# Kernel tuning notes

Measured on AMD Instinct MI355X. Metric: run time of the kernel, lower is better.

Reference implementation:

```python
import jax, jax.numpy as jnp
import numpy as np

SLOPE = 0.1  # supar MLP uses LeakyReLU(0.1)

def _mlp(x, W, b):
    return jax.nn.leaky_relu(x @ W + b, negative_slope=SLOPE)

def _triaffine(x, y, z, W):
    # supar Triaffine with n_out=1: s[b,z,x,y] = sum_{i,k,j} x[b,x,i] W[i,k,j] y[b,y,j] z[b,z,k]
    w = jnp.einsum('bzk,ikj->bzij', z, W)          # [b, n, d, d]
    return jnp.einsum('bxi,bzij,byj->bzxy', x, w, y)  # [b, n, n, n]

def _triu_sym(s):
    # s.triu() + s.triu(1).transpose(-1, -2) over last two dims
    return jnp.triu(s) + jnp.swapaxes(jnp.triu(s, 1), -1, -2)

def setup_inputs() -> dict:
    key = jax.random.key(0)
    B, N, D_IN, D = 2, 128, 1024, 150
    ks = jax.random.split(key, 16)
    sc_in = 1.0 / np.sqrt(D_IN)
    sc_tri = float(D) ** -1.5  # keeps triaffine outputs O(1)
    def nrm(k, shape, sc):
        return jax.random.normal(k, shape, jnp.float32) * sc
    return {
        'x':   jax.random.normal(ks[0], (B, N, D_IN), jnp.float32),
        'W_sh': nrm(ks[1], (D_IN, D), sc_in), 'b_sh': jnp.zeros((D,), jnp.float32),
        'W_st': nrm(ks[2], (D_IN, D), sc_in), 'b_st': jnp.zeros((D,), jnp.float32),
        'W_p':  nrm(ks[3], (D_IN, D), sc_in), 'b_p':  jnp.zeros((D,), jnp.float32),
        'T_pt':    nrm(ks[4], (D, D, D), sc_tri),
        'T_ph':    nrm(ks[5], (D, D, D), sc_tri),
        'T_phsib': nrm(ks[6], (D, D, D), sc_tri),
        'T_ptsib': nrm(ks[7], (D, D, D), sc_tri),
        'T_phcop': nrm(ks[8], (D, D, D), sc_tri),
        'T_ptcop': nrm(ks[9], (D, D, D), sc_tri),
    }

def reference(x, W_sh, b_sh, W_st, b_st, W_p, b_p,
              T_pt, T_ph, T_phsib, T_ptsib, T_phcop, T_ptcop):
    # eval mode: dropout is identity; ind_prd=False so p2 == p (shared MLP)
    sh = _mlp(x, W_sh, b_sh)
    st = _mlp(x, W_st, b_st)
    p = _mlp(x, W_p, b_p)
    p2 = p
    # span scores: [b, p, sh_idx, st_idx]
    span_pst = _triu_sym(_triaffine(sh, st, p2, T_pt))
    span_psh = _triaffine(sh, st, p, T_ph)
    # sibling scores: [b, p, h, h'] / [b, p, t, t']
    ph_sib = _triu_sym(_triaffine(sh, sh, p, T_phsib))
    pt_sib = _triu_sym(_triaffine(st, st, p2, T_ptsib))
    # co-parent scores: triaffine gives [b, h, p, p'], permute(0,2,3,1) -> [b, p, p', h]
    ph_cop = jnp.transpose(_triu_sym(_triaffine(p, p, sh, T_phcop)), (0, 2, 3, 1))
    pt_cop = jnp.transpose(_triu_sym(_triaffine(p2, p2, st, T_ptcop)), (0, 2, 3, 1))
    return (span_psh, span_pst, ph_sib, pt_sib, ph_cop, pt_cop)
```

## Files before the change

### kernel.cpp

```cpp
#include <hip/hip_runtime.h>


#define DD    150
#define KP    160
#define OUTBLK 4194304
#define NWZ   24064
#define TTG   3840000
#define WZG   (256*NWZ)
#define HROW  (256*160)

__device__ __forceinline__ unsigned short f2u(float f) {
  unsigned x = __float_as_uint(f);
  x += 0x7FFFu + ((x >> 16) & 1u);
  return (unsigned short)(x >> 16);
}

typedef __attribute__((ext_vector_type(8))) short frag8;
typedef __attribute__((ext_vector_type(4))) float facc4;

__constant__ int c_zsel[6] = {2, 2, 2, 2, 0, 1};
__constant__ int c_xsel[6] = {0, 0, 0, 1, 2, 2};
__constant__ int c_ysel[6] = {1, 1, 0, 1, 2, 2};

__global__ __launch_bounds__(256) void mlp_partial(
    const float* __restrict__ x,
    const float* __restrict__ W0, const float* __restrict__ W1, const float* __restrict__ W2,
    float* __restrict__ P)
{
  int m = blockIdx.x, bt = blockIdx.y, ks = blockIdx.z;
  const float* W = (m == 0) ? W0 : (m == 1) ? W1 : W2;
  int bn0 = bt * 32, k0 = ks * 128;
  __shared__ float xs[32][132];
  int tid = threadIdx.x;
  for (int e = 0; e < 4; ++e) {
    int l = e * 256 + tid;
    int row = l >> 5, c4 = l & 31;
    float4 v = *(const float4*)&x[(bn0 + row) * 1024 + k0 + c4 * 4];
    xs[row][c4 * 4 + 0] = v.x; xs[row][c4 * 4 + 1] = v.y;
    xs[row][c4 * 4 + 2] = v.z; xs[row][c4 * 4 + 3] = v.w;
  }
  __syncthreads();
  int tj = tid & 15, tt = tid >> 4, r = tt * 2;
  int dd[10];
  #pragma unroll
  for (int u = 0; u < 10; ++u) { int d = tj + 16 * u; dd[u] = d < 150 ? d : 149; }
  float a0[10], a1[10];
  #pragma unroll
  for (int u = 0; u < 10; ++u) { a0[u] = 0.f; a1[u] = 0.f; }
  for (int k = 0; k < 128; ++k) {
    float xa = xs[r][k], xb = xs[r + 1][k];
    const float* wr = W + (long long)(k0 + k) * 150;
    #pragma unroll
    for (int u = 0; u < 10; ++u) {
      float w = wr[dd[u]];
      a0[u] += xa * w; a1[u] += xb * w;
    }
  }
  float* Pb = P + (long long)(m * 8 + ks) * 256 * 160;
  #pragma unroll
  for (int u = 0; u < 10; ++u) {
    int d = tj + 16 * u;
    Pb[(bn0 + r) * 160 + d]     = a0[u];
    Pb[(bn0 + r + 1) * 160 + d] = a1[u];
  }
}

__global__ __launch_bounds__(256) void mlp_reduce(
    const float* __restrict__ P,
    const float* __restrict__ B0, const float* __restrict__ B1, const float* __restrict__ B2,
    unsigned short* __restrict__ H)
{
  int o = blockIdx.x * 256 + threadIdx.x;
  int d = o % 160;
  int bn = (o / 160) & 255;
  int m = o / (160 * 256);
  float v = 0.f;
  if (d < 150) {
    const float* Bv = (m == 0) ? B0 : (m == 1) ? B1 : B2;
    v = Bv[d];
    #pragma unroll
    for (int ks = 0; ks < 8; ++ks)
      v += P[((long long)(m * 8 + ks) * 256 + bn) * 160 + d];
    v = v > 0.f ? v : 0.1f * v;
  }
  H[o] = f2u(v);
}

struct TPtrs { const float* t[6]; };
__global__ __launch_bounds__(256) void tt_kernel(TPtrs tp, unsigned short* __restrict__ TT3)
{
  int i = blockIdx.x;
  int ky = blockIdx.y % 5, jy = blockIdx.y / 5;
  int k0 = ky * 32, j0 = jy * 32;
  int g = blockIdx.z;
  const float* T = tp.t[g];
  unsigned short* TT = TT3 + (long long)g * TTG;
  __shared__ float tl[32][33];
  int tid = threadIdx.x;
  #pragma unroll
  for (int e = 0; e < 4; ++e) {
    int l = e * 256 + tid;
    int r = l >> 5, c = l & 31;
    float v = 0.f;
    if (i < 150 && k0 + r < 150 && j0 + c < 150)
      v = T[i * 22500 + (k0 + r) * 150 + (j0 + c)];
    tl[r][c] = v;
  }
  __syncthreads();
  #pragma unroll
  for (int e = 0; e < 4; ++e) {
    int l = e * 256 + tid;
    int rr = l >> 5, cc = l & 31;
    if (j0 + rr < 150)
      TT[(long long)((j0 + rr) * 160 + i) * 160 + k0 + cc] = f2u(tl[cc][rr]);
  }
}

__global__ __launch_bounds__(256) void wz_gemm(
    const unsigned short* __restrict__ Hb, const unsigned short* __restrict__ TT3,
    unsigned short* __restrict__ wz3)
{
  constexpr int LR = 72;
  __shared__ unsigned short lA[128 * LR];
  __shared__ unsigned short lB[128 * LR];
  int g = blockIdx.z, tid = threadIdx.x;
  const unsigned short* Ab = Hb + c_zsel[g] * HROW + blockIdx.y * 128 * 160;
  const unsigned short* Bb = TT3 + (long long)g * TTG;
  int n0 = blockIdx.x * 128;
  int wave = tid >> 6, lane = tid & 63;
  int l15 = lane & 15, lq = lane >> 4;
  int mw = (wave & 1) * 64, nw = (wave >> 1) * 64;
  facc4 acc[4][4];
  #pragma unroll
  for (int i = 0; i < 4; ++i)
    #pragma unroll
    for (int j = 0; j < 4; ++j) acc[i][j] = (facc4){0.f, 0.f, 0.f, 0.f};
  for (int ch = 0; ch < 3; ++ch) {
    int k0 = ch << 6;
    int sh = (ch == 2) ? 2 : 3, upr = 1 << sh;
    for (int u = tid; u < 128 * upr; u += 256) {
      int row = u >> sh, off = (u & (upr - 1)) << 3;
      *(uint4*)&lA[row * LR + off] = *(const uint4*)&Ab[row * 160 + k0 + off];
    }
    for (int u = tid; u < 128 * upr; u += 256) {
      int row = u >> sh, off = (u & (upr - 1)) << 3;
      int gn = n0 + row;
      uint4 v; v.x = 0u; v.y = 0u; v.z = 0u; v.w = 0u;
      if (gn < 24000) v = *(const uint4*)&Bb[(long long)gn * 160 + k0 + off];
      *(uint4*)&lB[row * LR + off] = v;
    }
    __syncthreads();
    int nks = (ch == 2) ? 1 : 2;
    for (int ks = 0; ks < nks; ++ks) {
      int ko = (ks << 5) + (lq << 3);
      frag8 af[4], bf[4];
      #pragma unroll
      for (int i = 0; i < 4; ++i) af[i] = *(const frag8*)&lA[(mw + i * 16 + l15) * LR + ko];
      #pragma unroll
      for (int j = 0; j < 4; ++j) bf[j] = *(const frag8*)&lB[(nw + j * 16 + l15) * LR + ko];
      #pragma unroll
      for (int i = 0; i < 4; ++i)
        #pragma unroll
        for (int j = 0; j < 4; ++j)
          acc[i][j] = __builtin_amdgcn_mfma_f32_16x16x32_bf16(af[i], bf[j], acc[i][j], 0, 0, 0);
    }
    __syncthreads();
  }
  unsigned short* C = wz3 + (long long)g * WZG;
  int mb = blockIdx.y * 128 + mw;
  #pragma unroll
  for (int i = 0; i < 4; ++i)
    #pragma unroll
    for (int r = 0; r < 4; ++r) {
      int m = mb + i * 16 + lq * 4 + r;
      #pragma unroll
      for (int j = 0; j < 4; ++j)
        C[(long long)m * NWZ + n0 + nw + j * 16 + l15] = f2u(acc[i][j][r]);
    }
}

__global__ __launch_bounds__(256) void tmp_gemm(
    const unsigned short* __restrict__ Hb, const unsigned short* __restrict__ wz3,
    unsigned short* __restrict__ tmp3)
{
  constexpr int LR = 72;
  __shared__ unsigned short lA[128 * LR];
  __shared__ unsigned short lB[160 * LR];
  int z = blockIdx.x, tid = threadIdx.x;
  int g = z >> 8, bz = z & 255, b = bz >> 7;
  const unsigned short* Ab = Hb + c_xsel[g] * HROW + b * 128 * 160;
  const unsigned short* Bb = wz3 + (long long)g * WZG + (long long)bz * NWZ;
  int wave = tid >> 6, lane = tid & 63;
  int l15 = lane & 15, lq = lane >> 4;
  int mw = (wave & 1) * 64, nw = (wave >> 1) * 80;
  facc4 acc[4][5];
  #pragma unroll
  for (int i = 0; i < 4; ++i)
    #pragma unroll
    for (int j = 0; j < 5; ++j) acc[i][j] = (facc4){0.f, 0.f, 0.f, 0.f};
  for (int ch = 0; ch < 3; ++ch) {
    int k0 = ch << 6;
    int sh = (ch == 2) ? 2 : 3, upr = 1 << sh;
    for (int u = tid; u < 128 * upr; u += 256) {
      int row = u >> sh, off = (u & (upr - 1)) << 3;
      *(uint4*)&lA[row * LR + off] = *(const uint4*)&Ab[row * 160 + k0 + off];
    }
    for (int u = tid; u < 160 * upr; u += 256) {
      int row = u >> sh, off = (u & (upr - 1)) << 3;
      uint4 v; v.x = 0u; v.y = 0u; v.z = 0u; v.w = 0u;
      if (row < 150) v = *(const uint4*)&Bb[row * 160 + k0 + off];
      *(uint4*)&lB[row * LR + off] = v;
    }
    __syncthreads();
    int nks = (ch == 2) ? 1 : 2;
    for (int ks = 0; ks < nks; ++ks) {
      int ko = (ks << 5) + (lq << 3);
      frag8 af[4], bf[5];
      #pragma unroll
      for (int i = 0; i < 4; ++i) af[i] = *(const frag8*)&lA[(mw + i * 16 + l15) * LR + ko];
      #pragma unroll
      for (int j = 0; j < 5; ++j) bf[j] = *(const frag8*)&lB[(nw + j * 16 + l15) * LR + ko];
      #pragma unroll
      for (int i = 0; i < 4; ++i)
        #pragma unroll
        for (int j = 0; j < 5; ++j)
          acc[i][j] = __builtin_amdgcn_mfma_f32_16x16x32_bf16(af[i], bf[j], acc[i][j], 0, 0, 0);
    }
    __syncthreads();
  }
  unsigned short* C = tmp3 + (long long)z * (128 * 160);
  #pragma unroll
  for (int i = 0; i < 4; ++i)
    #pragma unroll
    for (int r = 0; r < 4; ++r) {
      int m = mw + i * 16 + lq * 4 + r;
      #pragma unroll
      for (int j = 0; j < 5; ++j)
        C[m * 160 + nw + j * 16 + l15] = f2u(acc[i][j][r]);
    }
}

struct SPtrs { float* p[6]; };
__global__ __launch_bounds__(256) void s_gemm(
    const unsigned short* __restrict__ tmp3, const unsigned short* __restrict__ Hb,
    SPtrs sp)
{
  constexpr int LR = 72;
  __shared__ unsigned short lA[128 * LR];
  __shared__ unsigned short lB[128 * LR];
  int z = blockIdx.x, tid = threadIdx.x;
  int g = z >> 8, bz = z & 255, b = bz >> 7;
  const unsigned short* Ab = tmp3 + (long long)z * (128 * 160);
  const unsigned short* Bb = Hb + c_ysel[g] * HROW + b * 128 * 160;
  int wave = tid >> 6, lane = tid & 63;
  int l15 = lane & 15, lq = lane >> 4;
  int mw = (wave & 1) * 64, nw = (wave >> 1) * 64;
  facc4 acc[4][4];
  #pragma unroll
  for (int i = 0; i < 4; ++i)
    #pragma unroll
    for (int j = 0; j < 4; ++j) acc[i][j] = (facc4){0.f, 0.f, 0.f, 0.f};
  for (int ch = 0; ch < 3; ++ch) {
    int k0 = ch << 6;
    int sh = (ch == 2) ? 2 : 3, upr = 1 << sh;
    for (int u = tid; u < 128 * upr; u += 256) {
      int row = u >> sh, off = (u & (upr - 1)) << 3;
      *(uint4*)&lA[row * LR + off] = *(const uint4*)&Ab[row * 160 + k0 + off];
      *(uint4*)&lB[row * LR + off] = *(const uint4*)&Bb[row * 160 + k0 + off];
    }
    __syncthreads();
    int nks = (ch == 2) ? 1 : 2;
    for (int ks = 0; ks < nks; ++ks) {
      int ko = (ks << 5) + (lq << 3);
      frag8 af[4], bf[4];
      #pragma unroll
      for (int i = 0; i < 4; ++i) af[i] = *(const frag8*)&lA[(mw + i * 16 + l15) * LR + ko];
      #pragma unroll
      for (int j = 0; j < 4; ++j) bf[j] = *(const frag8*)&lB[(nw + j * 16 + l15) * LR + ko];
      #pragma unroll
      for (int i = 0; i < 4; ++i)
        #pragma unroll
        for (int j = 0; j < 4; ++j)
          acc[i][j] = __builtin_amdgcn_mfma_f32_16x16x32_bf16(af[i], bf[j], acc[i][j], 0, 0, 0);
    }
    __syncthreads();
  }
  float* C = sp.p[g] + (long long)bz * 16384;
  #pragma unroll
  for (int i = 0; i < 4; ++i)
    #pragma unroll
    for (int r = 0; r < 4; ++r) {
      int m = mw + i * 16 + lq * 4 + r;
      #pragma unroll
      for (int j = 0; j < 4; ++j)
        C[m * 128 + nw + j * 16 + l15] = acc[i][j][r];
    }
}

__global__ __launch_bounds__(256) void sym_kernel(float* __restrict__ out)
{
  int idx = blockIdx.x * 256 + threadIdx.x;
  int grp = idx >> 22;
  int o = idx & (OUTBLK - 1);
  float* s = out + (long long)(1 + grp) * OUTBLK;
  int y = o & 127;
  int x = (o >> 7) & 127;
  if (x > y) {
    int bz = o >> 14;
    s[o] = s[(bz << 14) + (y << 7) + x];
  }
}

__global__ __launch_bounds__(256) void cop_kernel(
    const float* __restrict__ ss, float* __restrict__ out)
{
  int w0 = blockIdx.x << 5;
  int z0 = blockIdx.y << 5;
  int g  = blockIdx.z >> 1, b = blockIdx.z & 1;
  const float* sg = ss + (long long)g * OUTBLK;
  float* outp = out + (long long)(4 + g) * OUTBLK;
  __shared__ float tl[32][33];
  int tid = threadIdx.x;
  #pragma unroll
  for (int e = 0; e < 4; ++e) {
    int l = e * 256 + tid;
    int r = l >> 5, c = l & 31;
    int w = w0 + c;
    int xx = w >> 7, yy = w & 127;
    int sx = xx < yy ? xx : yy;
    int sy = xx < yy ? yy : xx;
    tl[r][c] = sg[(((b << 7) + z0 + r) << 14) + (sx << 7) + sy];
  }
  __syncthreads();
  #pragma unroll
  for (int e = 0; e < 4; ++e) {
    int l = e * 256 + tid;
    int rr = l >> 5, cc = l & 31;
    outp[(b << 21) + ((w0 + rr) << 7) + z0 + cc] = tl[cc][rr];
  }
}

extern "C" void kernel_launch(void* const* d_in, const int* in_sizes, int n_in,
                              void* d_out, int out_size, void* d_ws, size_t ws_size,
                              hipStream_t stream)
{
  const float* x   = (const float*)d_in[0];
  const float* Wsh = (const float*)d_in[1];
  const float* bsh = (const float*)d_in[2];
  const float* Wst = (const float*)d_in[3];
  const float* bst = (const float*)d_in[4];
  const float* Wp  = (const float*)d_in[5];
  const float* bp  = (const float*)d_in[6];
  TPtrs tp;
  tp.t[0] = (const float*)d_in[8];
  tp.t[1] = (const float*)d_in[7];
  tp.t[2] = (const float*)d_in[9];
  tp.t[3] = (const float*)d_in[10];
  tp.t[4] = (const float*)d_in[11];
  tp.t[5] = (const float*)d_in[12];
  float* out = (float*)d_out;
  char* wsb = (char*)d_ws;

  unsigned short* Hb   = (unsigned short*)(wsb);
  unsigned short* TT3  = (unsigned short*)(wsb + 245760);
  unsigned short* wz3  = (unsigned short*)(wsb + 46325760);
  unsigned short* tmp3 = (unsigned short*)(wsb + 120250368);
  float* P  = (float*)wz3;
  float* ss = (float*)TT3;

  SPtrs sp;
  sp.p[0] = out + 0LL * OUTBLK;
  sp.p[1] = out + 1LL * OUTBLK;
  sp.p[2] = out + 2LL * OUTBLK;
  sp.p[3] = out + 3LL * OUTBLK;
  sp.p[4] = ss;
  sp.p[5] = ss + OUTBLK;

  mlp_partial<<<dim3(3, 8, 8),   256, 0, stream>>>(x, Wsh, Wst, Wp, P);
  mlp_reduce <<<dim3(480),       256, 0, stream>>>(P, bsh, bst, bp, Hb);
  tt_kernel  <<<dim3(160, 25, 6),256, 0, stream>>>(tp, TT3);
  wz_gemm    <<<dim3(188, 2, 6), 256, 0, stream>>>(Hb, TT3, wz3);
  tmp_gemm   <<<dim3(1536),      256, 0, stream>>>(Hb, wz3, tmp3);
  s_gemm     <<<dim3(1536),      256, 0, stream>>>(tmp3, Hb, sp);
  sym_kernel <<<dim3(49152),     256, 0, stream>>>(out);
  cop_kernel <<<dim3(512, 4, 4), 256, 0, stream>>>(ss, out);
}
```

Before: 411.2 us.

## Fuse tmp and score GEMMs and fold triu symmetrization into epilogue

Merges the tmp_gemm and s_gemm kernels into one block-level kernel that keeps the intermediate bf16 tmp tile in shared memory instead of writing it to global memory and reading it back. For the symmetric score groups, the epilogue stages the tile in swizzled shared memory and writes the mirrored upper triangle directly, which removes the separate sym_kernel pass over three output tensors. The co-parent groups write only the upper triangle, since cop_kernel reads only that part. The larger shared-memory union (about 84 KB) may lower occupancy.

```diff
diff --git a/kernel.cpp b/kernel.cpp
--- a/kernel.cpp
+++ b/kernel.cpp
@@ -153,16 +153,16 @@
     int nks = (ch == 2) ? 1 : 2;
     for (int ks = 0; ks < nks; ++ks) {
       int ko = (ks << 5) + (lq << 3);
-      frag8 af[4], bf[4];
+      frag8 af[4], bfr[4];
       #pragma unroll
       for (int i = 0; i < 4; ++i) af[i] = *(const frag8*)&lA[(mw + i * 16 + l15) * LR + ko];
       #pragma unroll
-      for (int j = 0; j < 4; ++j) bf[j] = *(const frag8*)&lB[(nw + j * 16 + l15) * LR + ko];
+      for (int j = 0; j < 4; ++j) bfr[j] = *(const frag8*)&lB[(nw + j * 16 + l15) * LR + ko];
       #pragma unroll
       for (int i = 0; i < 4; ++i)
         #pragma unroll
         for (int j = 0; j < 4; ++j)
-          acc[i][j] = __builtin_amdgcn_mfma_f32_16x16x32_bf16(af[i], bf[j], acc[i][j], 0, 0, 0);
+          acc[i][j] = __builtin_amdgcn_mfma_f32_16x16x32_bf16(af[i], bfr[j], acc[i][j], 0, 0, 0);
     }
     __syncthreads();
   }
@@ -179,20 +179,26 @@
     }
 }
 
-__global__ __launch_bounds__(256) void tmp_gemm(
+struct SPtrs { float* p[6]; };
+__global__ __launch_bounds__(256) void tmps_gemm(
     const unsigned short* __restrict__ Hb, const unsigned short* __restrict__ wz3,
-    unsigned short* __restrict__ tmp3)
-{
-  constexpr int LR = 72;
-  __shared__ unsigned short lA[128 * LR];
-  __shared__ unsigned short lB[160 * LR];
+    SPtrs sp)
+{
+  __shared__ union {
+    struct { unsigned short A[128 * 72]; unsigned short B[160 * 72]; } p1;
+    struct { unsigned short T[128 * 168]; unsigned short B[128 * 72]; } p2;
+    float sq[128 * 128];
+  } sm;
+
   int z = blockIdx.x, tid = threadIdx.x;
   int g = z >> 8, bz = z & 255, b = bz >> 7;
   const unsigned short* Ab = Hb + c_xsel[g] * HROW + b * 128 * 160;
   const unsigned short* Bb = wz3 + (long long)g * WZG + (long long)bz * NWZ;
   int wave = tid >> 6, lane = tid & 63;
   int l15 = lane & 15, lq = lane >> 4;
-  int mw = (wave & 1) * 64, nw = (wave >> 1) * 80;
+  int mw = (wave & 1) * 64;
+  int nw80 = (wave >> 1) * 80, nw64 = (wave >> 1) * 64;
+
   facc4 acc[4][5];
   #pragma unroll
   for (int i = 0; i < 4; ++i)
@@ -203,32 +209,32 @@
     int sh = (ch == 2) ? 2 : 3, upr = 1 << sh;
     for (int u = tid; u < 128 * upr; u += 256) {
       int row = u >> sh, off = (u & (upr - 1)) << 3;
-      *(uint4*)&lA[row * LR + off] = *(const uint4*)&Ab[row * 160 + k0 + off];
+      *(uint4*)&sm.p1.A[row * 72 + off] = *(const uint4*)&Ab[row * 160 + k0 + off];
     }
     for (int u = tid; u < 160 * upr; u += 256) {
       int row = u >> sh, off = (u & (upr - 1)) << 3;
       uint4 v; v.x = 0u; v.y = 0u; v.z = 0u; v.w = 0u;
       if (row < 150) v = *(const uint4*)&Bb[row * 160 + k0 + off];
-      *(uint4*)&lB[row * LR + off] = v;
+      *(uint4*)&sm.p1.B[row * 72 + off] = v;
     }
     __syncthreads();
     int nks = (ch == 2) ? 1 : 2;
     for (int ks = 0; ks < nks; ++ks) {
       int ko = (ks << 5) + (lq << 3);
-      frag8 af[4], bf[5];
-      #pragma unroll
-      for (int i = 0; i < 4; ++i) af[i] = *(const frag8*)&lA[(mw + i * 16 + l15) * LR + ko];
-      #pragma unroll
-      for (int j = 0; j < 5; ++j) bf[j] = *(const frag8*)&lB[(nw + j * 16 + l15) * LR + ko];
+      frag8 af[4], bfr[5];
+      #pragma unroll
+      for (int i = 0; i < 4; ++i) af[i] = *(const frag8*)&sm.p1.A[(mw + i * 16 + l15) * 72 + ko];
+      #pragma unroll
+      for (int j = 0; j < 5; ++j) bfr[j] = *(const frag8*)&sm.p1.B[(nw80 + j * 16 + l15) * 72 + ko];
       #pragma unroll
       for (int i = 0; i < 4; ++i)
         #pragma unroll
         for (int j = 0; j < 5; ++j)
-          acc[i][j] = __builtin_amdgcn_mfma_f32_16x16x32_bf16(af[i], bf[j], acc[i][j], 0, 0, 0);
-    }
-    __syncthreads();
-  }
-  unsigned short* C = tmp3 + (long long)z * (128 * 160);
+          acc[i][j] = __builtin_amdgcn_mfma_f32_16x16x32_bf16(af[i], bfr[j], acc[i][j], 0, 0, 0);
+    }
+    __syncthreads();
+  }
+
   #pragma unroll
   for (int i = 0; i < 4; ++i)
     #pragma unroll
@@ -236,78 +242,92 @@
       int m = mw + i * 16 + lq * 4 + r;
       #pragma unroll
       for (int j = 0; j < 5; ++j)
-        C[m * 160 + nw + j * 16 + l15] = f2u(acc[i][j][r]);
-    }
-}
-
-struct SPtrs { float* p[6]; };
-__global__ __launch_bounds__(256) void s_gemm(
-    const unsigned short* __restrict__ tmp3, const unsigned short* __restrict__ Hb,
-    SPtrs sp)
-{
-  constexpr int LR = 72;
-  __shared__ unsigned short lA[128 * LR];
-  __shared__ unsigned short lB[128 * LR];
-  int z = blockIdx.x, tid = threadIdx.x;
-  int g = z >> 8, bz = z & 255, b = bz >> 7;
-  const unsigned short* Ab = tmp3 + (long long)z * (128 * 160);
-  const unsigned short* Bb = Hb + c_ysel[g] * HROW + b * 128 * 160;
-  int wave = tid >> 6, lane = tid & 63;
-  int l15 = lane & 15, lq = lane >> 4;
-  int mw = (wave & 1) * 64, nw = (wave >> 1) * 64;
-  facc4 acc[4][4];
+        sm.p2.T[m * 168 + nw80 + j * 16 + l15] = f2u(acc[i][j][r]);
+    }
+
+  const unsigned short* Yb = Hb + c_ysel[g] * HROW + b * 128 * 160;
+  facc4 acc2[4][4];
   #pragma unroll
   for (int i = 0; i < 4; ++i)
     #pragma unroll
-    for (int j = 0; j < 4; ++j) acc[i][j] = (facc4){0.f, 0.f, 0.f, 0.f};
+    for (int j = 0; j < 4; ++j) acc2[i][j] = (facc4){0.f, 0.f, 0.f, 0.f};
   for (int ch = 0; ch < 3; ++ch) {
     int k0 = ch << 6;
     int sh = (ch == 2) ? 2 : 3, upr = 1 << sh;
+    __syncthreads();
     for (int u = tid; u < 128 * upr; u += 256) {
       int row = u >> sh, off = (u & (upr - 1)) << 3;
-      *(uint4*)&lA[row * LR + off] = *(const uint4*)&Ab[row * 160 + k0 + off];
-      *(uint4*)&lB[row * LR + off] = *(const uint4*)&Bb[row * 160 + k0 + off];
+      *(uint4*)&sm.p2.B[row * 72 + off] = *(const uint4*)&Yb[row * 160 + k0 + off];
     }
     __syncthreads();
     int nks = (ch == 2) ? 1 : 2;
     for (int ks = 0; ks < nks; ++ks) {
       int ko = (ks << 5) + (lq << 3);
-      frag8 af[4], bf[4];
-      #pragma unroll
-      for (int i = 0; i < 4; ++i) af[i] = *(const frag8*)&lA[(mw + i * 16 + l15) * LR + ko];
-      #pragma unroll
-      for (int j = 0; j < 4; ++j) bf[j] = *(const frag8*)&lB[(nw + j * 16 + l15) * LR + ko];
+      frag8 af[4], bfr[4];
       #pragma unroll
       for (int i = 0; i < 4; ++i)
+        af[i] = *(const frag8*)&sm.p2.T[(mw + i * 16 + l15) * 168 + k0 + ko];
+      #pragma unroll
+      for (int j = 0; j < 4; ++j)
+        bfr[j] = *(const frag8*)&sm.p2.B[(nw64 + j * 16 + l15) * 72 + ko];
+      #pragma unroll
+      for (int i = 0; i < 4; ++i)
         #pragma unroll
         for (int j = 0; j < 4; ++j)
-          acc[i][j] = __builtin_amdgcn_mfma_f32_16x16x32_bf16(af[i], bf[j], acc[i][j], 0, 0, 0);
-    }
-    __syncthreads();
-  }
+          acc2[i][j] = __builtin_amdgcn_mfma_f32_16x16x32_bf16(af[i], bfr[j], acc2[i][j], 0, 0, 0);
+    }
+  }
+
   float* C = sp.p[g] + (long long)bz * 16384;
-  #pragma unroll
-  for (int i = 0; i < 4; ++i)
-    #pragma unroll
-    for (int r = 0; r < 4; ++r) {
-      int m = mw + i * 16 + lq * 4 + r;
-      #pragma unroll
-      for (int j = 0; j < 4; ++j)
-        C[m * 128 + nw + j * 16 + l15] = acc[i][j][r];
-    }
-}
-
-__global__ __launch_bounds__(256) void sym_kernel(float* __restrict__ out)
-{
-  int idx = blockIdx.x * 256 + threadIdx.x;
-  int grp = idx >> 22;
-  int o = idx & (OUTBLK - 1);
-  float* s = out + (long long)(1 + grp) * OUTBLK;
-  int y = o & 127;
-  int x = (o >> 7) & 127;
-  if (x > y) {
-    int bz = o >> 14;
-    s[o] = s[(bz << 14) + (y << 7) + x];
+  if (g >= 1 && g <= 3) {
+    __syncthreads();
+    #pragma unroll
+    for (int i = 0; i < 4; ++i)
+      #pragma unroll
+      for (int r = 0; r < 4; ++r) {
+        int m = mw + i * 16 + lq * 4 + r;
+        #pragma unroll
+        for (int j = 0; j < 4; ++j) {
+          int n = nw64 + j * 16 + l15;
+          sm.sq[m * 128 + (n ^ (m & 31))] = acc2[i][j][r];
+        }
+      }
+    __syncthreads();
+    #pragma unroll
+    for (int i = 0; i < 4; ++i)
+      #pragma unroll
+      for (int r = 0; r < 4; ++r) {
+        int m = mw + i * 16 + lq * 4 + r;
+        #pragma unroll
+        for (int j = 0; j < 4; ++j) {
+          int n = nw64 + j * 16 + l15;
+          int mn = m < n ? m : n;
+          int mx = m ^ n ^ mn;
+          C[m * 128 + n] = sm.sq[mn * 128 + (mx ^ (mn & 31))];
+        }
+      }
+  } else if (g == 0) {
+    #pragma unroll
+    for (int i = 0; i < 4; ++i)
+      #pragma unroll
+      for (int r = 0; r < 4; ++r) {
+        int m = mw + i * 16 + lq * 4 + r;
+        #pragma unroll
+        for (int j = 0; j < 4; ++j)
+          C[m * 128 + nw64 + j * 16 + l15] = acc2[i][j][r];
+      }
+  } else {
+    #pragma unroll
+    for (int i = 0; i < 4; ++i)
+      #pragma unroll
+      for (int r = 0; r < 4; ++r) {
+        int m = mw + i * 16 + lq * 4 + r;
+        #pragma unroll
+        for (int j = 0; j < 4; ++j) {
+          int n = nw64 + j * 16 + l15;
+          if (m <= n) C[m * 128 + n] = acc2[i][j][r];
+        }
+      }
   }
 }
 
@@ -364,7 +384,6 @@
   unsigned short* Hb   = (unsigned short*)(wsb);
   unsigned short* TT3  = (unsigned short*)(wsb + 245760);
   unsigned short* wz3  = (unsigned short*)(wsb + 46325760);
-  unsigned short* tmp3 = (unsigned short*)(wsb + 120250368);
   float* P  = (float*)wz3;
   float* ss = (float*)TT3;
 
@@ -376,12 +395,10 @@
   sp.p[4] = ss;
   sp.p[5] = ss + OUTBLK;
 
-  mlp_partial<<<dim3(3, 8, 8),   256, 0, stream>>>(x, Wsh, Wst, Wp, P);
-  mlp_reduce <<<dim3(480),       256, 0, stream>>>(P, bsh, bst, bp, Hb);
-  tt_kernel  <<<dim3(160, 25, 6),256, 0, stream>>>(tp, TT3);
-  wz_gemm    <<<dim3(188, 2, 6), 256, 0, stream>>>(Hb, TT3, wz3);
-  tmp_gemm   <<<dim3(1536),      256, 0, stream>>>(Hb, wz3, tmp3);
-  s_gemm     <<<dim3(1536),      256, 0, stream>>>(tmp3, Hb, sp);
-  sym_kernel <<<dim3(49152),     256, 0, stream>>>(out);
-  cop_kernel <<<dim3(512, 4, 4), 256, 0, stream>>>(ss, out);
-}
+  mlp_partial<<<dim3(3, 8, 8),    256, 0, stream>>>(x, Wsh, Wst, Wp, P);
+  mlp_reduce <<<dim3(480),        256, 0, stream>>>(P, bsh, bst, bp, Hb);
+  tt_kernel  <<<dim3(160, 25, 6), 256, 0, stream>>>(tp, TT3);
+  wz_gemm    <<<dim3(188, 2, 6),  256, 0, stream>>>(Hb, TT3, wz3);
+  tmps_gemm  <<<dim3(1536),       256, 0, stream>>>(Hb, wz3, sp);
+  cop_kernel <<<dim3(512, 4, 4),  256, 0, stream>>>(ss, out);
+}
```

Result: faster. 368.3 us (-10.4%).
